# Optimization experiments

Measured on AMD Instinct MI355X. Metric: run time of the kernel, lower is better.

## Reference

```python
import jax, jax.numpy as jnp
import numpy as np

B, N, E, R, D, L = 2, 40000, 400000, 64, 64, 6
LN_EPS = 1e-5


def _layer_norm(x, g, b):
    mu = jnp.mean(x, axis=-1, keepdims=True)
    var = jnp.var(x, axis=-1, keepdims=True)
    return (x - mu) * jax.lax.rsqrt(var + LN_EPS) * g + b


def setup_inputs() -> dict:
    key = jax.random.key(0)
    ks = jax.random.split(key, 10)
    s = 0.05
    return {
        "rel_reps": jax.random.normal(ks[0], (B, R, D), jnp.float32),
        "h_index": jax.random.randint(ks[1], (B,), 0, N, jnp.int32),
        "r_index": jax.random.randint(ks[2], (B,), 0, R, jnp.int32),
        "edge_index": jax.random.randint(ks[3], (2, E), 0, N, jnp.int32),
        "edge_type": jax.random.randint(ks[4], (E,), 0, R, jnp.int32),
        "proj_w1": jax.random.normal(ks[5], (L, D, D), jnp.float32) * s,
        "proj_b1": jnp.zeros((L, D), jnp.float32),
        "proj_w2": jax.random.normal(ks[6], (L, D, D), jnp.float32) * s,
        "proj_b2": jnp.zeros((L, D), jnp.float32),
        "lin_w": jax.random.normal(ks[7], (L, 2 * D, D), jnp.float32) * s,
        "lin_b": jnp.zeros((L, D), jnp.float32),
        "ln_g": jnp.ones((L, D), jnp.float32),
        "ln_b": jnp.zeros((L, D), jnp.float32),
        "mlp_w": jax.random.normal(ks[8], (2 * D, 2 * D), jnp.float32) * s,
        "mlp_b": jnp.zeros((2 * D,), jnp.float32),
        "num_nodes": N,
    }


def reference(rel_reps, h_index, r_index, edge_index, edge_type,
              proj_w1, proj_b1, proj_w2, proj_b2,
              lin_w, lin_b, ln_g, ln_b, mlp_w, mlp_b, num_nodes):
    # EntityNBFNet.bellmanford with 6 GeneralizedRelationalConv layers
    # (distmult message, sum aggregate, layer_norm, relu, short_cut).
    batch = rel_reps.shape[0]
    query = rel_reps[jnp.arange(batch), r_index]                     # [B, D]
    boundary = jnp.zeros((batch, num_nodes, rel_reps.shape[-1]), rel_reps.dtype)
    boundary = boundary.at[jnp.arange(batch), h_index].set(query)    # [B, N, D]
    src, dst = edge_index[0], edge_index[1]

    def layer_step(x, params):
        pw1, pb1, pw2, pb2, lw, lb, lng, lnb = params
        # per-layer relation projection MLP (project_relations=True)
        rel = jax.nn.relu(jnp.einsum("brd,de->bre", rel_reps, pw1) + pb1)
        rel = jnp.einsum("brd,de->bre", rel, pw2) + pb2              # [B, R, D]
        # distmult message: x_src * rel_edge  -> [B, E, D]
        msg = jnp.take(x, src, axis=1) * jnp.take(rel, edge_type, axis=1)
        # sum aggregation (edge_weight = ones) + boundary self-message
        agg = jax.vmap(lambda m: jax.ops.segment_sum(m, dst, num_segments=num_nodes))(msg)
        agg = agg + boundary
        out = jnp.concatenate([x, agg], axis=-1) @ lw + lb           # [B, N, D]
        out = jax.nn.relu(_layer_norm(out, lng, lnb))
        out = out + x                                                # short cut
        return out, None

    x, _ = jax.lax.scan(layer_step, boundary,
                        (proj_w1, proj_b1, proj_w2, proj_b2, lin_w, lin_b, ln_g, ln_b))
    node_query = jnp.broadcast_to(query[:, None, :], x.shape)        # [B, N, D]
    feature = jnp.concatenate([x, node_query], axis=-1)              # [B, N, 2D]
    # embedd_out=True: MLP = Linear(2D, 2D) + ReLU
    embedd = jax.nn.relu(feature @ mlp_w + mlp_b)
    return embedd
```

## Files before the change

### kernel.cpp

```cpp
#include <hip/hip_runtime.h>
#include <hip/hip_bf16.h>

namespace {

constexpr int B = 2;
constexpr int N = 40000;
constexpr int E = 400000;
constexpr int R = 64;
constexpr int D = 64;
constexpr int L = 6;
constexpr float EPS = 1e-5f;
constexpr int NB = (N + 255) / 256;
constexpr int EB = (E + 255) / 256;

typedef _Float16 v8h __attribute__((ext_vector_type(8)));
typedef _Float16 v2h __attribute__((ext_vector_type(2)));
typedef float    v4f __attribute__((ext_vector_type(4)));

__device__ __forceinline__ unsigned int pack_h2(float a, float b) {
  v2h p; p.x = (_Float16)a; p.y = (_Float16)b;
  return __builtin_bit_cast(unsigned int, p);
}
__device__ __forceinline__ float2 unpack_h2(unsigned int u) {
  v2h p = __builtin_bit_cast(v2h, u);
  return make_float2((float)p.x, (float)p.y);
}


__global__ void k_init(const float* __restrict__ rel_reps,
                       const int* __restrict__ h_index, const int* __restrict__ r_index,
                       unsigned int* __restrict__ xb,
                       _Float16* __restrict__ xrow0, _Float16* __restrict__ xrow1,
                       float* __restrict__ query_f, _Float16* __restrict__ qh) {
  int d = threadIdx.x;
  int h0 = h_index[0], h1 = h_index[1];
  float q0 = rel_reps[r_index[0] * D + d];
  float q1 = rel_reps[(R + r_index[1]) * D + d];
  query_f[d * 2] = q0; query_f[d * 2 + 1] = q1;
  qh[d]     = (_Float16)q0;
  qh[D + d] = (_Float16)q1;
  if (h0 == h1) {
    xb[(size_t)h0 * D + d] = pack_h2(q0, q1);
  } else {
    xb[(size_t)h0 * D + d] = pack_h2(q0, 0.f);
    xb[(size_t)h1 * D + d] = pack_h2(0.f, q1);
  }
  xrow0[(size_t)h0 * 2 * D + d] = (_Float16)q0;
  xrow1[(size_t)h1 * 2 * D + d] = (_Float16)q1;
}

__global__ __launch_bounds__(64) void k_rel(
    const float* __restrict__ rel_reps,
    const float* __restrict__ pw1, const float* __restrict__ pb1,
    const float* __restrict__ pw2, const float* __restrict__ pb2,
    float* __restrict__ rel_f) {
  __shared__ float row[D];
  __shared__ float row2[D];
  int idx = blockIdx.x;
  int l = idx / (B * R);
  int br = idx - l * (B * R);
  int b = br / R, r = br - b * R;
  int d = threadIdx.x;
  row[d] = rel_reps[(size_t)br * D + d];
  __syncthreads();
  const float* w1 = pw1 + (size_t)l * D * D;
  float acc = pb1[l * D + d];
  for (int k = 0; k < D; ++k) acc = fmaf(row[k], w1[k * D + d], acc);
  row2[d] = fmaxf(acc, 0.f);
  __syncthreads();
  const float* w2 = pw2 + (size_t)l * D * D;
  float acc2 = pb2[l * D + d];
  for (int k = 0; k < D; ++k) acc2 = fmaf(row2[k], w2[k * D + d], acc2);
  rel_f[(((size_t)l * R + r) * D + d) * 2 + b] = acc2;
}

__global__ __launch_bounds__(256) void k_pack_rel(const float2* __restrict__ rel2,
                                                  unsigned int* __restrict__ rel_pk) {
  int i = blockIdx.x * 256 + threadIdx.x;
  if (i < L * R * D) {
    float2 v = rel2[i];
    rel_pk[i] = pack_h2(v.x, v.y);
  }
}

__global__ __launch_bounds__(64) void k_pack_w(const float* __restrict__ lin_w,
                                               unsigned short* __restrict__ Wf) {
  int idx = blockIdx.x;
  int l = idx >> 4;
  int ct = (idx >> 2) & 3, ks = idx & 3;
  int lane = threadIdx.x;
  int n = ct * 16 + (lane & 15);
  #pragma unroll
  for (int j = 0; j < 8; ++j) {
    int k = ks * 32 + (lane >> 4) * 8 + j;
    _Float16 v = (_Float16)lin_w[(size_t)l * 2 * D * D + (size_t)k * D + n];
    Wf[(size_t)l * 8192 + ((size_t)(ct * 4 + ks) * 64 + lane) * 8 + j] =
        __builtin_bit_cast(unsigned short, v);
  }
}

__global__ __launch_bounds__(64) void k_pack_wm(const float* __restrict__ mlp_w,
                                                unsigned short* __restrict__ Wm) {
  int idx = blockIdx.x;
  int ct = idx >> 2, ks = idx & 3;
  int lane = threadIdx.x;
  int n = ct * 16 + (lane & 15);
  #pragma unroll
  for (int j = 0; j < 8; ++j) {
    int k = ks * 32 + (lane >> 4) * 8 + j;
    _Float16 v = (_Float16)mlp_w[(size_t)k * 2 * D + n];
    Wm[((size_t)idx * 64 + lane) * 8 + j] = __builtin_bit_cast(unsigned short, v);
  }
}

__global__ __launch_bounds__(256) void k_hist(const int* __restrict__ dst,
                                              int* __restrict__ cnt) {
  int e = blockIdx.x * 256 + threadIdx.x;
  if (e < E) atomicAdd(&cnt[dst[e]], 1);
}

__global__ __launch_bounds__(256) void k_scan1(const int* __restrict__ cnt,
                                               int* __restrict__ row_ptr,
                                               int* __restrict__ bsum) {
  __shared__ int s[256];
  int t = threadIdx.x;
  int i = blockIdx.x * 256 + t;
  int v = (i < N) ? cnt[i] : 0;
  s[t] = v;
  __syncthreads();
  #pragma unroll
  for (int off = 1; off < 256; off <<= 1) {
    int u = (t >= off) ? s[t - off] : 0;
    __syncthreads();
    s[t] += u;
    __syncthreads();
  }
  if (i < N) row_ptr[i] = s[t] - v;
  if (t == 255) bsum[blockIdx.x] = s[255];
}

__global__ __launch_bounds__(256) void k_scan2(int* __restrict__ bsum,
                                               int* __restrict__ row_ptr) {
  __shared__ int s[NB];
  int t = threadIdx.x;
  if (t < NB) s[t] = bsum[t];
  __syncthreads();
  if (t == 0) {
    int run = 0;
    for (int i = 0; i < NB; ++i) { int v = s[i]; s[i] = run; run += v; }
    row_ptr[N] = run;
  }
  __syncthreads();
  if (t < NB) bsum[t] = s[t];
}

__global__ __launch_bounds__(256) void k_scan3(int* __restrict__ row_ptr,
                                               const int* __restrict__ bsum,
                                               int* __restrict__ cursor) {
  int i = blockIdx.x * 256 + threadIdx.x;
  if (i < N) {
    int v = row_ptr[i] + bsum[blockIdx.x];
    row_ptr[i] = v;
    cursor[i] = v;
  }
}

__global__ __launch_bounds__(256) void k_fill(const int* __restrict__ src,
                                              const int* __restrict__ dst,
                                              const int* __restrict__ etype,
                                              int* __restrict__ cursor,
                                              unsigned int* __restrict__ es) {
  int e = blockIdx.x * 256 + threadIdx.x;
  if (e < E) {
    int p = atomicAdd(&cursor[dst[e]], 1);
    es[p] = (unsigned int)src[e] | ((unsigned int)etype[e] << 16);
  }
}

__global__ __launch_bounds__(256, 8) void k_gather(
    const unsigned int* __restrict__ xb,
    _Float16* __restrict__ xrow0, _Float16* __restrict__ xrow1,
    const unsigned int* __restrict__ rel_pk,
    const int* __restrict__ row_ptr, const unsigned int* __restrict__ es,
    const float2* __restrict__ q2, const int* __restrict__ h_index, int first) {
  int tid = threadIdx.x;
  int lane = tid & 63;
  int h = lane >> 5;
  int ln = lane & 31;
  int w = (blockIdx.x * 256 + tid) >> 6;
  int n = w * 2 + h;
  int h0 = h_index[0], h1 = h_index[1];
  int rp = 0;
  if (lane < 3) rp = row_ptr[2 * w + lane];
  int rs = __shfl(rp, h);
  int re = __shfl(rp, h + 1);
  int deg = re - rs;
  int dc = min(deg, 32);
  unsigned int esv = 0;
  if (ln < dc) esv = es[rs + ln];
  float a0x = 0.f, a0y = 0.f, a1x = 0.f, a1y = 0.f;
  if (first) {
    for (int j = 0; j < dc; ++j) {
      unsigned int pk = __shfl(esv, (h << 5) | j);
      int s = (int)(pk & 0xffffu), et = (int)(pk >> 16);
      if (s == h0 || s == h1) {
        uint2 xv = *(const uint2*)&xb[(size_t)s * D + 2 * ln];
        uint2 rv = *(const uint2*)&rel_pk[et * D + 2 * ln];
        float2 xfx = unpack_h2(xv.x), xfy = unpack_h2(xv.y);
        float2 rfx = unpack_h2(rv.x), rfy = unpack_h2(rv.y);
        if (s == h0) { a0x = fmaf(xfx.x, rfx.x, a0x); a0y = fmaf(xfy.x, rfy.x, a0y); }
        if (s == h1) { a1x = fmaf(xfx.y, rfx.y, a1x); a1y = fmaf(xfy.y, rfy.y, a1y); }
      }
    }
    for (int j = rs + 32; j < re; ++j) {
      unsigned int pk = es[j];
      int s = (int)(pk & 0xffffu), et = (int)(pk >> 16);
      if (s == h0 || s == h1) {
        uint2 xv = *(const uint2*)&xb[(size_t)s * D + 2 * ln];
        uint2 rv = *(const uint2*)&rel_pk[et * D + 2 * ln];
        float2 xfx = unpack_h2(xv.x), xfy = unpack_h2(xv.y);
        float2 rfx = unpack_h2(rv.x), rfy = unpack_h2(rv.y);
        if (s == h0) { a0x = fmaf(xfx.x, rfx.x, a0x); a0y = fmaf(xfy.x, rfy.x, a0y); }
        if (s == h1) { a1x = fmaf(xfx.y, rfx.y, a1x); a1y = fmaf(xfy.y, rfy.y, a1y); }
      }
    }
  } else {
    int rounds = (dc + 3) >> 2;
    int maxr = max(__shfl(rounds, 0), __shfl(rounds, 32));
    for (int jr = 0; jr < maxr; ++jr) {
      int j = jr * 4;
      int i0 = max(min(j + 0, dc - 1), 0), i1 = max(min(j + 1, dc - 1), 0);
      int i2 = max(min(j + 2, dc - 1), 0), i3 = max(min(j + 3, dc - 1), 0);
      unsigned int p0 = __shfl(esv, (h << 5) | i0);
      unsigned int p1 = __shfl(esv, (h << 5) | i1);
      unsigned int p2 = __shfl(esv, (h << 5) | i2);
      unsigned int p3 = __shfl(esv, (h << 5) | i3);
      uint2 xv0 = *(const uint2*)&xb[(size_t)(p0 & 0xffffu) * D + 2 * ln];
      uint2 xv1 = *(const uint2*)&xb[(size_t)(p1 & 0xffffu) * D + 2 * ln];
      uint2 xv2 = *(const uint2*)&xb[(size_t)(p2 & 0xffffu) * D + 2 * ln];
      uint2 xv3 = *(const uint2*)&xb[(size_t)(p3 & 0xffffu) * D + 2 * ln];
      uint2 rv0 = *(const uint2*)&rel_pk[(p0 >> 16) * D + 2 * ln];
      uint2 rv1 = *(const uint2*)&rel_pk[(p1 >> 16) * D + 2 * ln];
      uint2 rv2 = *(const uint2*)&rel_pk[(p2 >> 16) * D + 2 * ln];
      uint2 rv3 = *(const uint2*)&rel_pk[(p3 >> 16) * D + 2 * ln];
      if (j + 0 < dc) {
        float2 xfx = unpack_h2(xv0.x), xfy = unpack_h2(xv0.y);
        float2 rfx = unpack_h2(rv0.x), rfy = unpack_h2(rv0.y);
        a0x = fmaf(xfx.x, rfx.x, a0x); a1x = fmaf(xfx.y, rfx.y, a1x);
        a0y = fmaf(xfy.x, rfy.x, a0y); a1y = fmaf(xfy.y, rfy.y, a1y);
      }
      if (j + 1 < dc) {
        float2 xfx = unpack_h2(xv1.x), xfy = unpack_h2(xv1.y);
        float2 rfx = unpack_h2(rv1.x), rfy = unpack_h2(rv1.y);
        a0x = fmaf(xfx.x, rfx.x, a0x); a1x = fmaf(xfx.y, rfx.y, a1x);
        a0y = fmaf(xfy.x, rfy.x, a0y); a1y = fmaf(xfy.y, rfy.y, a1y);
      }
      if (j + 2 < dc) {
        float2 xfx = unpack_h2(xv2.x), xfy = unpack_h2(xv2.y);
        float2 rfx = unpack_h2(rv2.x), rfy = unpack_h2(rv2.y);
        a0x = fmaf(xfx.x, rfx.x, a0x); a1x = fmaf(xfx.y, rfx.y, a1x);
        a0y = fmaf(xfy.x, rfy.x, a0y); a1y = fmaf(xfy.y, rfy.y, a1y);
      }
      if (j + 3 < dc) {
        float2 xfx = unpack_h2(xv3.x), xfy = unpack_h2(xv3.y);
        float2 rfx = unpack_h2(rv3.x), rfy = unpack_h2(rv3.y);
        a0x = fmaf(xfx.x, rfx.x, a0x); a1x = fmaf(xfx.y, rfx.y, a1x);
        a0y = fmaf(xfy.x, rfy.x, a0y); a1y = fmaf(xfy.y, rfy.y, a1y);
      }
    }
    for (int j = rs + 32; j < re; ++j) {
      unsigned int pk = es[j];
      uint2 xv = *(const uint2*)&xb[(size_t)(pk & 0xffffu) * D + 2 * ln];
      uint2 rv = *(const uint2*)&rel_pk[(pk >> 16) * D + 2 * ln];
      float2 xfx = unpack_h2(xv.x), xfy = unpack_h2(xv.y);
      float2 rfx = unpack_h2(rv.x), rfy = unpack_h2(rv.y);
      a0x = fmaf(xfx.x, rfx.x, a0x); a1x = fmaf(xfx.y, rfx.y, a1x);
      a0y = fmaf(xfy.x, rfy.x, a0y); a1y = fmaf(xfy.y, rfy.y, a1y);
    }
  }
  if (n == h0) {
    float4 qq = *(const float4*)&q2[2 * ln];
    a0x += qq.x; a0y += qq.z;
  }
  if (n == h1) {
    float4 qq = *(const float4*)&q2[2 * ln];
    a1x += qq.y; a1y += qq.w;
  }
  v2h s0; s0.x = (_Float16)a0x; s0.y = (_Float16)a0y;
  v2h s1; s1.x = (_Float16)a1x; s1.y = (_Float16)a1y;
  *(v2h*)&xrow0[(size_t)n * 2 * D + D + 2 * ln] = s0;
  *(v2h*)&xrow1[(size_t)n * 2 * D + D + 2 * ln] = s1;
}

__global__ __launch_bounds__(64) void k_linear(
    unsigned int* __restrict__ xb,
    _Float16* __restrict__ xrow0, _Float16* __restrict__ xrow1,
    const unsigned short* __restrict__ Wf,
    const float* __restrict__ lin_b, const float* __restrict__ ln_g,
    const float* __restrict__ ln_b, int layer) {
  int lane = threadIdx.x;
  int nb = blockIdx.x * 16;
  int c = lane & 15, rg = lane >> 4;
  const v8h* wf = (const v8h*)(Wf + (size_t)layer * 8192);
  v8h Bf[4][4];
  #pragma unroll
  for (int ct = 0; ct < 4; ++ct)
    #pragma unroll
    for (int ks = 0; ks < 4; ++ks)
      Bf[ct][ks] = wf[(ct * 4 + ks) * 64 + lane];
  v4f acc0[4], acc1[4];
  #pragma unroll
  for (int ct = 0; ct < 4; ++ct) {
    acc0[ct] = (v4f){0.f, 0.f, 0.f, 0.f};
    acc1[ct] = (v4f){0.f, 0.f, 0.f, 0.f};
  }
  #pragma unroll
  for (int ks = 0; ks < 4; ++ks) {
    size_t aoff = (size_t)(nb + c) * 2 * D + ks * 32 + rg * 8;
    v8h A0 = *(const v8h*)(xrow0 + aoff);
    v8h A1 = *(const v8h*)(xrow1 + aoff);
    #pragma unroll
    for (int ct = 0; ct < 4; ++ct) {
      acc0[ct] = __builtin_amdgcn_mfma_f32_16x16x32_f16(A0, Bf[ct][ks], acc0[ct], 0, 0, 0);
      acc1[ct] = __builtin_amdgcn_mfma_f32_16x16x32_f16(A1, Bf[ct][ks], acc1[ct], 0, 0, 0);
    }
  }
  float bias4[4], g4[4], be4[4];
  #pragma unroll
  for (int ct = 0; ct < 4; ++ct) {
    int d = ct * 16 + c;
    bias4[ct] = lin_b[layer * D + d];
    g4[ct]    = ln_g[layer * D + d];
    be4[ct]   = ln_b[layer * D + d];
  }
  #pragma unroll
  for (int j = 0; j < 4; ++j) {
    int node = nb + rg * 4 + j;
    float v0[4], v1[4];
    float s10 = 0.f, s20 = 0.f, s11 = 0.f, s21 = 0.f;
    #pragma unroll
    for (int ct = 0; ct < 4; ++ct) {
      v0[ct] = acc0[ct][j] + bias4[ct];
      v1[ct] = acc1[ct][j] + bias4[ct];
      s10 += v0[ct]; s20 += v0[ct] * v0[ct];
      s11 += v1[ct]; s21 += v1[ct] * v1[ct];
    }
    #pragma unroll
    for (int mk = 1; mk < 16; mk <<= 1) {
      s10 += __shfl_xor(s10, mk); s20 += __shfl_xor(s20, mk);
      s11 += __shfl_xor(s11, mk); s21 += __shfl_xor(s21, mk);
    }
    float mu0 = s10 * (1.f / D), var0 = s20 * (1.f / D) - mu0 * mu0;
    float mu1 = s11 * (1.f / D), var1 = s21 * (1.f / D) - mu1 * mu1;
    float rs0 = rsqrtf(var0 + EPS), rs1 = rsqrtf(var1 + EPS);
    #pragma unroll
    for (int ct = 0; ct < 4; ++ct) {
      int d = ct * 16 + c;
      float o0 = fmaxf((v0[ct] - mu0) * rs0 * g4[ct] + be4[ct], 0.f);
      float o1 = fmaxf((v1[ct] - mu1) * rs1 * g4[ct] + be4[ct], 0.f);
      float2 xv = unpack_h2(xb[(size_t)node * D + d]);
      float r0 = o0 + xv.x, r1 = o1 + xv.y;
      xb[(size_t)node * D + d] = pack_h2(r0, r1);
      xrow0[(size_t)node * 2 * D + d] = (_Float16)r0;
      xrow1[(size_t)node * 2 * D + d] = (_Float16)r1;
    }
  }
}

__global__ __launch_bounds__(64) void k_mlp(
    const _Float16* __restrict__ xrow0, const _Float16* __restrict__ xrow1,
    const _Float16* __restrict__ qh,
    const unsigned short* __restrict__ Wm,
    const float* __restrict__ mlp_b,
    float* __restrict__ outf) {
  int lane = threadIdx.x;
  int nb = blockIdx.x * 16;
  int c = lane & 15, rg = lane >> 4;
  const v8h* wm = (const v8h*)Wm;
  v4f acc0[8], acc1[8];
  #pragma unroll
  for (int ct = 0; ct < 8; ++ct) {
    acc0[ct] = (v4f){0.f, 0.f, 0.f, 0.f};
    acc1[ct] = (v4f){0.f, 0.f, 0.f, 0.f};
  }
  #pragma unroll
  for (int ks = 0; ks < 4; ++ks) {
    v8h A0, A1;
    if (ks < 2) {
      size_t aoff = (size_t)(nb + c) * 2 * D + ks * 32 + rg * 8;
      A0 = *(const v8h*)(xrow0 + aoff);
      A1 = *(const v8h*)(xrow1 + aoff);
    } else {
      int qoff = (ks - 2) * 32 + rg * 8;
      A0 = *(const v8h*)(qh + qoff);
      A1 = *(const v8h*)(qh + D + qoff);
    }
    #pragma unroll
    for (int ct = 0; ct < 8; ++ct) {
      v8h Bv = wm[(ct * 4 + ks) * 64 + lane];
      acc0[ct] = __builtin_amdgcn_mfma_f32_16x16x32_f16(A0, Bv, acc0[ct], 0, 0, 0);
      acc1[ct] = __builtin_amdgcn_mfma_f32_16x16x32_f16(A1, Bv, acc1[ct], 0, 0, 0);
    }
  }
  #pragma unroll
  for (int ct = 0; ct < 8; ++ct) {
    int d = ct * 16 + c;
    float bias = mlp_b[d];
    #pragma unroll
    for (int j = 0; j < 4; ++j) {
      int node = nb + rg * 4 + j;
      outf[(size_t)node * 2 * D + d]       = fmaxf(acc0[ct][j] + bias, 0.f);
      outf[((size_t)N + node) * 2 * D + d] = fmaxf(acc1[ct][j] + bias, 0.f);
    }
  }
}

}

extern "C" void kernel_launch(void* const* d_in, const int* in_sizes, int n_in,
                              void* d_out, int out_size, void* d_ws, size_t ws_size,
                              hipStream_t stream) {
  const float* rel_reps = (const float*)d_in[0];
  const int* h_index    = (const int*)d_in[1];
  const int* r_index    = (const int*)d_in[2];
  const int* edge_index = (const int*)d_in[3];
  const int* edge_type  = (const int*)d_in[4];
  const float* proj_w1  = (const float*)d_in[5];
  const float* proj_b1  = (const float*)d_in[6];
  const float* proj_w2  = (const float*)d_in[7];
  const float* proj_b2  = (const float*)d_in[8];
  const float* lin_w    = (const float*)d_in[9];
  const float* lin_b    = (const float*)d_in[10];
  const float* ln_g     = (const float*)d_in[11];
  const float* ln_b     = (const float*)d_in[12];
  const float* mlp_w    = (const float*)d_in[13];
  const float* mlp_b    = (const float*)d_in[14];

  float* rel_all = (float*)d_ws;
  float* query   = rel_all + (size_t)2 * L * R * D;
  int*   cnt     = (int*)(query + 2 * D);
  int*   row_ptr = cnt + N;
  int*   cursor  = row_ptr + (N + 1);
  unsigned int* es  = (unsigned int*)(cursor + N);
  int*   bsum    = (int*)(es + E);
  unsigned int* xb = (unsigned int*)(bsum + NB);
  unsigned int* rel_pk = xb + (size_t)N * D;
  unsigned short* Wf = (unsigned short*)(rel_pk + (size_t)L * R * D);
  _Float16* xrow0 = (_Float16*)(Wf + (size_t)L * 8192);
  _Float16* xrow1 = xrow0 + (size_t)N * 2 * D;
  unsigned short* Wm = (unsigned short*)(xrow1 + (size_t)N * 2 * D);
  _Float16* qh = (_Float16*)(Wm + 16384);

  const int* srcp = edge_index;
  const int* dstp = edge_index + E;

  hipMemsetAsync(xb, 0, (size_t)N * D * sizeof(unsigned int), stream);
  hipMemsetAsync(xrow0, 0, (size_t)N * 2 * D * sizeof(_Float16) * 2, stream);
  hipMemsetAsync(cnt, 0, N * sizeof(int), stream);
  k_init<<<1, 64, 0, stream>>>(rel_reps, h_index, r_index,
                               xb, xrow0, xrow1, query, qh);
  k_rel<<<L * B * R, 64, 0, stream>>>(rel_reps, proj_w1, proj_b1, proj_w2, proj_b2, rel_all);
  k_pack_rel<<<(L * R * D + 255) / 256, 256, 0, stream>>>((const float2*)rel_all, rel_pk);
  k_pack_w<<<L * 16, 64, 0, stream>>>(lin_w, Wf);
  k_pack_wm<<<32, 64, 0, stream>>>(mlp_w, Wm);
  k_hist<<<EB, 256, 0, stream>>>(dstp, cnt);
  k_scan1<<<NB, 256, 0, stream>>>(cnt, row_ptr, bsum);
  k_scan2<<<1, 256, 0, stream>>>(bsum, row_ptr);
  k_scan3<<<NB, 256, 0, stream>>>(row_ptr, bsum, cursor);
  k_fill<<<EB, 256, 0, stream>>>(srcp, dstp, edge_type, cursor, es);

  for (int l = 0; l < L; ++l) {
    k_gather<<<N / 8, 256, 0, stream>>>(xb, xrow0, xrow1,
                                        rel_pk + (size_t)l * R * D,
                                        row_ptr, es, (const float2*)query, h_index,
                                        (l == 0) ? 1 : 0);
    k_linear<<<N / 16, 64, 0, stream>>>(xb, xrow0, xrow1,
                                        Wf, lin_b, ln_g, ln_b, l);
  }
  k_mlp<<<N / 16, 64, 0, stream>>>(xrow0, xrow1, qh, Wm, mlp_b, (float*)d_out);
}
```

Measured before the change: 376.3 us.

## Merge setup kernels, fold scan pass, deepen gather unroll, and lower gather occupancy bound

Folds k_init into an extra k_rel block and the three pack kernels into one k_pack launch. k_scan2 is dropped: each k_scan3 block now reduces the preceding block sums itself, and row_ptr[N] is set to E directly. The memsets are merged by reordering the workspace layout. The gather inner loop goes from 4 to 8 edges per round to put more loads in flight, and its launch bound is relaxed from 8 to 6 waves. The extra in-flight loads raise register pressure and may lower occupancy.

```diff
diff --git a/kernel.cpp b/kernel.cpp
--- a/kernel.cpp
+++ b/kernel.cpp
@@ -27,40 +27,39 @@
 }
 
 
-__global__ void k_init(const float* __restrict__ rel_reps,
-                       const int* __restrict__ h_index, const int* __restrict__ r_index,
-                       unsigned int* __restrict__ xb,
-                       _Float16* __restrict__ xrow0, _Float16* __restrict__ xrow1,
-                       float* __restrict__ query_f, _Float16* __restrict__ qh) {
-  int d = threadIdx.x;
-  int h0 = h_index[0], h1 = h_index[1];
-  float q0 = rel_reps[r_index[0] * D + d];
-  float q1 = rel_reps[(R + r_index[1]) * D + d];
-  query_f[d * 2] = q0; query_f[d * 2 + 1] = q1;
-  qh[d]     = (_Float16)q0;
-  qh[D + d] = (_Float16)q1;
-  if (h0 == h1) {
-    xb[(size_t)h0 * D + d] = pack_h2(q0, q1);
-  } else {
-    xb[(size_t)h0 * D + d] = pack_h2(q0, 0.f);
-    xb[(size_t)h1 * D + d] = pack_h2(0.f, q1);
-  }
-  xrow0[(size_t)h0 * 2 * D + d] = (_Float16)q0;
-  xrow1[(size_t)h1 * 2 * D + d] = (_Float16)q1;
-}
-
 __global__ __launch_bounds__(64) void k_rel(
     const float* __restrict__ rel_reps,
     const float* __restrict__ pw1, const float* __restrict__ pb1,
     const float* __restrict__ pw2, const float* __restrict__ pb2,
-    float* __restrict__ rel_f) {
+    float* __restrict__ rel_f,
+    const int* __restrict__ h_index, const int* __restrict__ r_index,
+    unsigned int* __restrict__ xb,
+    _Float16* __restrict__ xrow0, _Float16* __restrict__ xrow1,
+    float* __restrict__ query_f, _Float16* __restrict__ qh) {
   __shared__ float row[D];
   __shared__ float row2[D];
   int idx = blockIdx.x;
+  int d = threadIdx.x;
+  if (idx == L * B * R) {
+    int h0 = h_index[0], h1 = h_index[1];
+    float q0 = rel_reps[r_index[0] * D + d];
+    float q1 = rel_reps[(R + r_index[1]) * D + d];
+    query_f[d * 2] = q0; query_f[d * 2 + 1] = q1;
+    qh[d]     = (_Float16)q0;
+    qh[D + d] = (_Float16)q1;
+    if (h0 == h1) {
+      xb[(size_t)h0 * D + d] = pack_h2(q0, q1);
+    } else {
+      xb[(size_t)h0 * D + d] = pack_h2(q0, 0.f);
+      xb[(size_t)h1 * D + d] = pack_h2(0.f, q1);
+    }
+    xrow0[(size_t)h0 * 2 * D + d] = (_Float16)q0;
+    xrow1[(size_t)h1 * 2 * D + d] = (_Float16)q1;
+    return;
+  }
   int l = idx / (B * R);
   int br = idx - l * (B * R);
   int b = br / R, r = br - b * R;
-  int d = threadIdx.x;
   row[d] = rel_reps[(size_t)br * D + d];
   __syncthreads();
   const float* w1 = pw1 + (size_t)l * D * D;
@@ -74,42 +73,39 @@
   rel_f[(((size_t)l * R + r) * D + d) * 2 + b] = acc2;
 }
 
-__global__ __launch_bounds__(256) void k_pack_rel(const float2* __restrict__ rel2,
-                                                  unsigned int* __restrict__ rel_pk) {
-  int i = blockIdx.x * 256 + threadIdx.x;
-  if (i < L * R * D) {
+__global__ __launch_bounds__(256) void k_pack(
+    const float2* __restrict__ rel2, unsigned int* __restrict__ rel_pk,
+    const float* __restrict__ lin_w, unsigned short* __restrict__ Wf,
+    const float* __restrict__ mlp_w, unsigned short* __restrict__ Wm) {
+  int blk = blockIdx.x;
+  int tid = threadIdx.x;
+  if (blk < 96) {
+    int i = blk * 256 + tid;
     float2 v = rel2[i];
     rel_pk[i] = pack_h2(v.x, v.y);
-  }
-}
-
-__global__ __launch_bounds__(64) void k_pack_w(const float* __restrict__ lin_w,
-                                               unsigned short* __restrict__ Wf) {
-  int idx = blockIdx.x;
-  int l = idx >> 4;
-  int ct = (idx >> 2) & 3, ks = idx & 3;
-  int lane = threadIdx.x;
-  int n = ct * 16 + (lane & 15);
-  #pragma unroll
-  for (int j = 0; j < 8; ++j) {
-    int k = ks * 32 + (lane >> 4) * 8 + j;
-    _Float16 v = (_Float16)lin_w[(size_t)l * 2 * D * D + (size_t)k * D + n];
-    Wf[(size_t)l * 8192 + ((size_t)(ct * 4 + ks) * 64 + lane) * 8 + j] =
-        __builtin_bit_cast(unsigned short, v);
-  }
-}
-
-__global__ __launch_bounds__(64) void k_pack_wm(const float* __restrict__ mlp_w,
-                                                unsigned short* __restrict__ Wm) {
-  int idx = blockIdx.x;
-  int ct = idx >> 2, ks = idx & 3;
-  int lane = threadIdx.x;
-  int n = ct * 16 + (lane & 15);
-  #pragma unroll
-  for (int j = 0; j < 8; ++j) {
-    int k = ks * 32 + (lane >> 4) * 8 + j;
-    _Float16 v = (_Float16)mlp_w[(size_t)k * 2 * D + n];
-    Wm[((size_t)idx * 64 + lane) * 8 + j] = __builtin_bit_cast(unsigned short, v);
+  } else if (blk < 120) {
+    int idx = (blk - 96) * 4 + (tid >> 6);
+    int lane = tid & 63;
+    int l = idx >> 4, ct = (idx >> 2) & 3, ks = idx & 3;
+    int n = ct * 16 + (lane & 15);
+    #pragma unroll
+    for (int j = 0; j < 8; ++j) {
+      int k = ks * 32 + (lane >> 4) * 8 + j;
+      _Float16 v = (_Float16)lin_w[(size_t)l * 2 * D * D + (size_t)k * D + n];
+      Wf[(size_t)l * 8192 + ((size_t)((ct * 4 + ks) * 64) + lane) * 8 + j] =
+          __builtin_bit_cast(unsigned short, v);
+    }
+  } else {
+    int idx = (blk - 120) * 4 + (tid >> 6);
+    int lane = tid & 63;
+    int ct = idx >> 2, ks = idx & 3;
+    int n = ct * 16 + (lane & 15);
+    #pragma unroll
+    for (int j = 0; j < 8; ++j) {
+      int k = ks * 32 + (lane >> 4) * 8 + j;
+      _Float16 v = (_Float16)mlp_w[(size_t)k * 2 * D + n];
+      Wm[((size_t)idx * 64 + lane) * 8 + j] = __builtin_bit_cast(unsigned short, v);
+    }
   }
 }
 
@@ -139,30 +135,27 @@
   if (t == 255) bsum[blockIdx.x] = s[255];
 }
 
-__global__ __launch_bounds__(256) void k_scan2(int* __restrict__ bsum,
-                                               int* __restrict__ row_ptr) {
-  __shared__ int s[NB];
-  int t = threadIdx.x;
-  if (t < NB) s[t] = bsum[t];
-  __syncthreads();
-  if (t == 0) {
-    int run = 0;
-    for (int i = 0; i < NB; ++i) { int v = s[i]; s[i] = run; run += v; }
-    row_ptr[N] = run;
-  }
-  __syncthreads();
-  if (t < NB) bsum[t] = s[t];
-}
-
 __global__ __launch_bounds__(256) void k_scan3(int* __restrict__ row_ptr,
                                                const int* __restrict__ bsum,
                                                int* __restrict__ cursor) {
-  int i = blockIdx.x * 256 + threadIdx.x;
+  __shared__ int red[256];
+  int t = threadIdx.x;
+  int v = (t < (int)blockIdx.x) ? bsum[t] : 0;
+  red[t] = v;
+  __syncthreads();
+  #pragma unroll
+  for (int off = 128; off > 0; off >>= 1) {
+    if (t < off) red[t] += red[t + off];
+    __syncthreads();
+  }
+  int offv = red[0];
+  int i = blockIdx.x * 256 + t;
   if (i < N) {
-    int v = row_ptr[i] + bsum[blockIdx.x];
-    row_ptr[i] = v;
-    cursor[i] = v;
-  }
+    int r = row_ptr[i] + offv;
+    row_ptr[i] = r;
+    cursor[i] = r;
+  }
+  if (i == N - 1) row_ptr[N] = E;
 }
 
 __global__ __launch_bounds__(256) void k_fill(const int* __restrict__ src,
@@ -177,7 +170,7 @@
   }
 }
 
-__global__ __launch_bounds__(256, 8) void k_gather(
+__global__ __launch_bounds__(256, 6) void k_gather(
     const unsigned int* __restrict__ xb,
     _Float16* __restrict__ xrow0, _Float16* __restrict__ xrow1,
     const unsigned int* __restrict__ rel_pk,
@@ -225,47 +218,30 @@
       }
     }
   } else {
-    int rounds = (dc + 3) >> 2;
+    int rounds = (dc + 7) >> 3;
     int maxr = max(__shfl(rounds, 0), __shfl(rounds, 32));
     for (int jr = 0; jr < maxr; ++jr) {
-      int j = jr * 4;
-      int i0 = max(min(j + 0, dc - 1), 0), i1 = max(min(j + 1, dc - 1), 0);
-      int i2 = max(min(j + 2, dc - 1), 0), i3 = max(min(j + 3, dc - 1), 0);
-      unsigned int p0 = __shfl(esv, (h << 5) | i0);
-      unsigned int p1 = __shfl(esv, (h << 5) | i1);
-      unsigned int p2 = __shfl(esv, (h << 5) | i2);
-      unsigned int p3 = __shfl(esv, (h << 5) | i3);
-      uint2 xv0 = *(const uint2*)&xb[(size_t)(p0 & 0xffffu) * D + 2 * ln];
-      uint2 xv1 = *(const uint2*)&xb[(size_t)(p1 & 0xffffu) * D + 2 * ln];
-      uint2 xv2 = *(const uint2*)&xb[(size_t)(p2 & 0xffffu) * D + 2 * ln];
-      uint2 xv3 = *(const uint2*)&xb[(size_t)(p3 & 0xffffu) * D + 2 * ln];
-      uint2 rv0 = *(const uint2*)&rel_pk[(p0 >> 16) * D + 2 * ln];
-      uint2 rv1 = *(const uint2*)&rel_pk[(p1 >> 16) * D + 2 * ln];
-      uint2 rv2 = *(const uint2*)&rel_pk[(p2 >> 16) * D + 2 * ln];
-      uint2 rv3 = *(const uint2*)&rel_pk[(p3 >> 16) * D + 2 * ln];
-      if (j + 0 < dc) {
-        float2 xfx = unpack_h2(xv0.x), xfy = unpack_h2(xv0.y);
-        float2 rfx = unpack_h2(rv0.x), rfy = unpack_h2(rv0.y);
-        a0x = fmaf(xfx.x, rfx.x, a0x); a1x = fmaf(xfx.y, rfx.y, a1x);
-        a0y = fmaf(xfy.x, rfy.x, a0y); a1y = fmaf(xfy.y, rfy.y, a1y);
+      int j = jr * 8;
+      unsigned int pk[8];
+      uint2 xv[8], rv[8];
+      #pragma unroll
+      for (int u = 0; u < 8; ++u) {
+        int iu = max(min(j + u, dc - 1), 0);
+        pk[u] = __shfl(esv, (h << 5) | iu);
       }
-      if (j + 1 < dc) {
-        float2 xfx = unpack_h2(xv1.x), xfy = unpack_h2(xv1.y);
-        float2 rfx = unpack_h2(rv1.x), rfy = unpack_h2(rv1.y);
-        a0x = fmaf(xfx.x, rfx.x, a0x); a1x = fmaf(xfx.y, rfx.y, a1x);
-        a0y = fmaf(xfy.x, rfy.x, a0y); a1y = fmaf(xfy.y, rfy.y, a1y);
+      #pragma unroll
+      for (int u = 0; u < 8; ++u) {
+        xv[u] = *(const uint2*)&xb[(size_t)(pk[u] & 0xffffu) * D + 2 * ln];
+        rv[u] = *(const uint2*)&rel_pk[(pk[u] >> 16) * D + 2 * ln];
       }
-      if (j + 2 < dc) {
-        float2 xfx = unpack_h2(xv2.x), xfy = unpack_h2(xv2.y);
-        float2 rfx = unpack_h2(rv2.x), rfy = unpack_h2(rv2.y);
-        a0x = fmaf(xfx.x, rfx.x, a0x); a1x = fmaf(xfx.y, rfx.y, a1x);
-        a0y = fmaf(xfy.x, rfy.x, a0y); a1y = fmaf(xfy.y, rfy.y, a1y);
-      }
-      if (j + 3 < dc) {
-        float2 xfx = unpack_h2(xv3.x), xfy = unpack_h2(xv3.y);
-        float2 rfx = unpack_h2(rv3.x), rfy = unpack_h2(rv3.y);
-        a0x = fmaf(xfx.x, rfx.x, a0x); a1x = fmaf(xfx.y, rfx.y, a1x);
-        a0y = fmaf(xfy.x, rfy.x, a0y); a1y = fmaf(xfy.y, rfy.y, a1y);
+      #pragma unroll
+      for (int u = 0; u < 8; ++u) {
+        if (j + u < dc) {
+          float2 xfx = unpack_h2(xv[u].x), xfy = unpack_h2(xv[u].y);
+          float2 rfx = unpack_h2(rv[u].x), rfy = unpack_h2(rv[u].y);
+          a0x = fmaf(xfx.x, rfx.x, a0x); a1x = fmaf(xfx.y, rfx.y, a1x);
+          a0y = fmaf(xfy.x, rfy.x, a0y); a1y = fmaf(xfy.y, rfy.y, a1y);
+        }
       }
     }
     for (int j = rs + 32; j < re; ++j) {
@@ -436,36 +412,32 @@
   const float* mlp_w    = (const float*)d_in[13];
   const float* mlp_b    = (const float*)d_in[14];
 
-  float* rel_all = (float*)d_ws;
+  unsigned int* xb = (unsigned int*)d_ws;
+  _Float16* xrow0 = (_Float16*)(xb + (size_t)N * D);
+  _Float16* xrow1 = xrow0 + (size_t)N * 2 * D;
+  unsigned int* rel_pk = (unsigned int*)(xrow1 + (size_t)N * 2 * D);
+  unsigned short* Wf = (unsigned short*)(rel_pk + (size_t)L * R * D);
+  unsigned short* Wm = Wf + (size_t)L * 8192;
+  _Float16* qh = (_Float16*)(Wm + 16384);
+  float* rel_all = (float*)(qh + 128);
   float* query   = rel_all + (size_t)2 * L * R * D;
   int*   cnt     = (int*)(query + 2 * D);
   int*   row_ptr = cnt + N;
   int*   cursor  = row_ptr + (N + 1);
-  unsigned int* es  = (unsigned int*)(cursor + N);
+  unsigned int* es = (unsigned int*)(cursor + N);
   int*   bsum    = (int*)(es + E);
-  unsigned int* xb = (unsigned int*)(bsum + NB);
-  unsigned int* rel_pk = xb + (size_t)N * D;
-  unsigned short* Wf = (unsigned short*)(rel_pk + (size_t)L * R * D);
-  _Float16* xrow0 = (_Float16*)(Wf + (size_t)L * 8192);
-  _Float16* xrow1 = xrow0 + (size_t)N * 2 * D;
-  unsigned short* Wm = (unsigned short*)(xrow1 + (size_t)N * 2 * D);
-  _Float16* qh = (_Float16*)(Wm + 16384);
 
   const int* srcp = edge_index;
   const int* dstp = edge_index + E;
 
-  hipMemsetAsync(xb, 0, (size_t)N * D * sizeof(unsigned int), stream);
-  hipMemsetAsync(xrow0, 0, (size_t)N * 2 * D * sizeof(_Float16) * 2, stream);
+  hipMemsetAsync(xb, 0, (size_t)N * D * 4 + (size_t)N * 2 * D * 2 * 2, stream);
   hipMemsetAsync(cnt, 0, N * sizeof(int), stream);
-  k_init<<<1, 64, 0, stream>>>(rel_reps, h_index, r_index,
-                               xb, xrow0, xrow1, query, qh);
-  k_rel<<<L * B * R, 64, 0, stream>>>(rel_reps, proj_w1, proj_b1, proj_w2, proj_b2, rel_all);
-  k_pack_rel<<<(L * R * D + 255) / 256, 256, 0, stream>>>((const float2*)rel_all, rel_pk);
-  k_pack_w<<<L * 16, 64, 0, stream>>>(lin_w, Wf);
-  k_pack_wm<<<32, 64, 0, stream>>>(mlp_w, Wm);
+  k_rel<<<L * B * R + 1, 64, 0, stream>>>(rel_reps, proj_w1, proj_b1, proj_w2, proj_b2,
+                                          rel_all, h_index, r_index,
+                                          xb, xrow0, xrow1, query, qh);
+  k_pack<<<128, 256, 0, stream>>>((const float2*)rel_all, rel_pk, lin_w, Wf, mlp_w, Wm);
   k_hist<<<EB, 256, 0, stream>>>(dstp, cnt);
   k_scan1<<<NB, 256, 0, stream>>>(cnt, row_ptr, bsum);
-  k_scan2<<<1, 256, 0, stream>>>(bsum, row_ptr);
   k_scan3<<<NB, 256, 0, stream>>>(row_ptr, bsum, cursor);
   k_fill<<<EB, 256, 0, stream>>>(srcp, dstp, edge_type, cursor, es);
 
```

Result: faster. 347.0 us (-7.8%).
